# Optimization experiments

Hardware: AMD Instinct MI355X
Metric: run time of the kernel (lower is better)

The kernel has to match this reference:

```python
import jax, jax.numpy as jnp
import numpy as np


def setup_inputs() -> dict:
    key = jax.random.key(0)
    k1, k2, k3, k4 = jax.random.split(key, 4)
    N, E, C_in, C_out = 100000, 1600000, 256, 128
    x = jax.random.normal(k1, (N, C_in), dtype=jnp.float32)
    edge_index = jax.random.randint(k2, (2, E), 0, N, dtype=jnp.int64)
    W = jax.random.normal(k3, (C_in, C_out), dtype=jnp.float32) * 0.05
    b = jax.random.normal(k4, (C_out,), dtype=jnp.float32) * 0.05
    return {"x": x, "edge_index": edge_index, "W": W, "b": b}


def reference(x, edge_index, W, b):
    # GCNConv (PyG defaults): add self-loops, symmetric normalization,
    # linear transform, scatter-sum aggregation, bias; then ReLU (norm=None).
    N = x.shape[0]
    loops = jnp.arange(N, dtype=edge_index.dtype)
    src = jnp.concatenate([edge_index[0], loops])  # [E+N] message sources (x_j)
    dst = jnp.concatenate([edge_index[1], loops])  # [E+N] aggregation targets

    deg = jax.ops.segment_sum(jnp.ones_like(dst, dtype=x.dtype), dst, num_segments=N)
    deg_inv_sqrt = jnp.where(deg > 0, jax.lax.rsqrt(jnp.maximum(deg, 1.0)), 0.0)
    norm = deg_inv_sqrt[src] * deg_inv_sqrt[dst]  # [E+N]

    h = x @ W                                      # [N, C_out]
    msg = h[src] * norm[:, None]                   # [E+N, C_out] gather + scale
    out = jax.ops.segment_sum(msg, dst, num_segments=N) + b  # scatter-add
    return jax.nn.relu(out)
```

## Files before the change

kernel.cpp:

```cpp
#include <hip/hip_runtime.h>


typedef __attribute__((ext_vector_type(8))) short bf16x8;
typedef __attribute__((ext_vector_type(4))) float f32x4;

__device__ __forceinline__ unsigned short f2bf(float f) {
  unsigned int u = __float_as_uint(f);
  u += 0x7FFFu + ((u >> 16) & 1u);
  return (unsigned short)(u >> 16);
}
__device__ __forceinline__ float bfval(unsigned short h) {
  return __uint_as_float(((unsigned int)h) << 16);
}
__device__ __forceinline__ float bf0(unsigned int u) { return __uint_as_float(u << 16); }
__device__ __forceinline__ float bf1(unsigned int u) { return __uint_as_float(u & 0xFFFF0000u); }

__global__ __launch_bounds__(256) void k_wprep(
    const float* __restrict__ W, unsigned short* __restrict__ blob,
    unsigned int* __restrict__ cnt, int N)
{
  int g = blockIdx.x * 256 + threadIdx.x;
  if (g < N) cnt[g] = 0u;
  if (g >= 256 * 128) return;
  int k = g >> 7, c = g & 127;
  float w = W[g];
  unsigned short hi = f2bf(w);
  unsigned short lo = f2bf(w - bfval(hi));
  int q = k >> 5, kk = k & 31;
  unsigned lin = (unsigned)(c * 64 + kk * 2);
  unsigned swz = lin ^ (((unsigned)(c & 7)) << 4);
  blob[(q * 16384 + swz) >> 1] = hi;
  blob[(q * 16384 + 8192 + swz) >> 1] = lo;
}

__global__ __launch_bounds__(256) void k_gemm_scatter(
    const float* __restrict__ x, const unsigned char* __restrict__ wblob,
    unsigned short* __restrict__ h, int N,
    const int* __restrict__ src, const int* __restrict__ dst,
    unsigned int* __restrict__ cnt, int* __restrict__ srcs, int E,
    int gemmB, int scatB)
{
  __shared__ __align__(16) unsigned char smem[20480];

  const int id = blockIdx.x;
  bool isGemm;
  int idx;
  if (scatB == 2 * gemmB) {
    if (id % 3 == 0) { isGemm = true;  idx = id / 3; }
    else             { isGemm = false; idx = id - 1 - id / 3; }
  } else {
    isGemm = id < gemmB;
    idx = isGemm ? id : id - gemmB;
  }

  const int tid = threadIdx.x;

  if (!isGemm) {
    if (idx < scatB) {
      int e = idx * 256 + tid;
      if (e < E) {
        int d = __builtin_nontemporal_load(dst + e);
        int s = __builtin_nontemporal_load(src + e);
        int pos = (int)atomicAdd(&cnt[d], 1u);
        if (pos < 64) __builtin_nontemporal_store(s, srcs + (((size_t)d << 6) + pos));
      }
    }
    return;
  }
  if (idx >= gemmB) return;

  const int row0 = idx * 32;
  const int lane = tid & 63;
  const int wv = tid >> 6;
  const int mb = wv & 1;
  const int nb = wv >> 1;

  f32x4 acc[4] = {};

  const int ar = tid >> 3;
  const int akk0 = (tid & 7) * 4;
  int arow = row0 + ar; if (arow >= N) arow = N - 1;
  const unsigned aaddr = ((unsigned)(ar * 64 + akk0 * 2)) ^ (((unsigned)(ar & 7)) << 4);

  const int rr = 16 * mb + (lane & 15);
  const unsigned aoff = ((unsigned)(rr * 64 + (lane >> 4) * 16)) ^ (((unsigned)(rr & 7)) << 4);

  for (int q = 0; q < 8; ++q) {
    {
      const f32x4 v = __builtin_nontemporal_load(
          (const f32x4*)(x + (size_t)arow * 256 + q * 32 + akk0));
      unsigned short h0 = f2bf(v[0]), h1 = f2bf(v[1]), h2 = f2bf(v[2]), h3 = f2bf(v[3]);
      unsigned short l0 = f2bf(v[0] - bfval(h0));
      unsigned short l1 = f2bf(v[1] - bfval(h1));
      unsigned short l2 = f2bf(v[2] - bfval(h2));
      unsigned short l3 = f2bf(v[3] - bfval(h3));
      *(uint2*)(smem + 16384 + aaddr) =
          make_uint2((unsigned)h0 | ((unsigned)h1 << 16), (unsigned)h2 | ((unsigned)h3 << 16));
      *(uint2*)(smem + 18432 + aaddr) =
          make_uint2((unsigned)l0 | ((unsigned)l1 << 16), (unsigned)l2 | ((unsigned)l3 << 16));
    }
    {
      const uint4* gb = (const uint4*)(wblob + (size_t)q * 16384);
      uint4* sb = (uint4*)smem;
      uint4 t0 = gb[tid], t1 = gb[tid + 256], t2 = gb[tid + 512], t3 = gb[tid + 768];
      sb[tid] = t0; sb[tid + 256] = t1; sb[tid + 512] = t2; sb[tid + 768] = t3;
    }
    __syncthreads();
    {
      const bf16x8 ah = *(const bf16x8*)(smem + 16384 + aoff);
      const bf16x8 al = *(const bf16x8*)(smem + 18432 + aoff);
      #pragma unroll
      for (int nf = 0; nf < 4; ++nf) {
        const int c = 64 * nb + 16 * nf + (lane & 15);
        const unsigned boff =
            ((unsigned)(c * 64 + (lane >> 4) * 16)) ^ (((unsigned)(c & 7)) << 4);
        const bf16x8 bh = *(const bf16x8*)(smem + boff);
        const bf16x8 bl = *(const bf16x8*)(smem + 8192 + boff);
        acc[nf] = __builtin_amdgcn_mfma_f32_16x16x32_bf16(ah, bh, acc[nf], 0, 0, 0);
        acc[nf] = __builtin_amdgcn_mfma_f32_16x16x32_bf16(ah, bl, acc[nf], 0, 0, 0);
        acc[nf] = __builtin_amdgcn_mfma_f32_16x16x32_bf16(al, bh, acc[nf], 0, 0, 0);
      }
    }
    __syncthreads();
  }

  #pragma unroll
  for (int nf = 0; nf < 4; ++nf) {
    const int col = 64 * nb + 16 * nf + (lane & 15);
    #pragma unroll
    for (int r = 0; r < 4; ++r) {
      const int row = row0 + 16 * mb + 4 * (lane >> 4) + r;
      if (row < N) h[(size_t)row * 128 + col] = f2bf(acc[nf][r]);
    }
  }
}

__global__ __launch_bounds__(256) void k_aggr(
    const unsigned short* __restrict__ h, const int* __restrict__ srcs,
    const unsigned int* __restrict__ cnt,
    const float* __restrict__ b, float* __restrict__ out, int N)
{
  const int wid = (int)(((size_t)blockIdx.x * 256 + threadIdx.x) >> 6);
  if (wid >= N) return;
  const int lane = threadIdx.x & 63;
  const int eg = lane >> 4;
  const int cl = lane & 15;
  const int deg = min((int)cnt[wid], 64);
  const int m = deg + 1;
  const size_t coff = (size_t)(cl << 3);
  const size_t lbase = (size_t)wid << 6;

  float a0 = 0.f, a1 = 0.f, a2 = 0.f, a3 = 0.f, a4 = 0.f, a5 = 0.f, a6 = 0.f, a7 = 0.f;

  for (int base = 0; base < m; base += 64) {
    const int kk = min(64, m - base);
    const int slot = base + lane;
    int sidx = wid;
    if (slot < deg) sidx = srcs[lbase + slot];
    const float sd = rsqrtf((float)(cnt[sidx] + 1u));
    int j = 0;
    for (; j + 8 <= kk; j += 8) {
      const int s0 = __shfl(sidx, j + eg, 64);
      const int s1 = __shfl(sidx, j + 4 + eg, 64);
      const float d0 = __shfl(sd, j + eg, 64);
      const float d1 = __shfl(sd, j + 4 + eg, 64);
      const uint4 v0 = *(const uint4*)(h + ((size_t)s0 << 7) + coff);
      const uint4 v1 = *(const uint4*)(h + ((size_t)s1 << 7) + coff);
      a0 = fmaf(bf0(v0.x), d0, a0); a1 = fmaf(bf1(v0.x), d0, a1);
      a2 = fmaf(bf0(v0.y), d0, a2); a3 = fmaf(bf1(v0.y), d0, a3);
      a4 = fmaf(bf0(v0.z), d0, a4); a5 = fmaf(bf1(v0.z), d0, a5);
      a6 = fmaf(bf0(v0.w), d0, a6); a7 = fmaf(bf1(v0.w), d0, a7);
      a0 = fmaf(bf0(v1.x), d1, a0); a1 = fmaf(bf1(v1.x), d1, a1);
      a2 = fmaf(bf0(v1.y), d1, a2); a3 = fmaf(bf1(v1.y), d1, a3);
      a4 = fmaf(bf0(v1.z), d1, a4); a5 = fmaf(bf1(v1.z), d1, a5);
      a6 = fmaf(bf0(v1.w), d1, a6); a7 = fmaf(bf1(v1.w), d1, a7);
    }
    for (; j < kk; j += 4) {
      const int s0 = __shfl(sidx, j + eg, 64);
      const float d0 = __shfl(sd, j + eg, 64);
      if (j + eg < kk) {
        const uint4 v0 = *(const uint4*)(h + ((size_t)s0 << 7) + coff);
        a0 = fmaf(bf0(v0.x), d0, a0); a1 = fmaf(bf1(v0.x), d0, a1);
        a2 = fmaf(bf0(v0.y), d0, a2); a3 = fmaf(bf1(v0.y), d0, a3);
        a4 = fmaf(bf0(v0.z), d0, a4); a5 = fmaf(bf1(v0.z), d0, a5);
        a6 = fmaf(bf0(v0.w), d0, a6); a7 = fmaf(bf1(v0.w), d0, a7);
      }
    }
  }

  a0 += __shfl_xor(a0, 16, 64); a0 += __shfl_xor(a0, 32, 64);
  a1 += __shfl_xor(a1, 16, 64); a1 += __shfl_xor(a1, 32, 64);
  a2 += __shfl_xor(a2, 16, 64); a2 += __shfl_xor(a2, 32, 64);
  a3 += __shfl_xor(a3, 16, 64); a3 += __shfl_xor(a3, 32, 64);
  a4 += __shfl_xor(a4, 16, 64); a4 += __shfl_xor(a4, 32, 64);
  a5 += __shfl_xor(a5, 16, 64); a5 += __shfl_xor(a5, 32, 64);
  a6 += __shfl_xor(a6, 16, 64); a6 += __shfl_xor(a6, 32, 64);
  a7 += __shfl_xor(a7, 16, 64); a7 += __shfl_xor(a7, 32, 64);

  if (lane < 32) {
    const float dn = rsqrtf((float)m);
    const int hi = lane >> 4;
    const int c0 = ((lane & 15) << 3) + (hi << 2);
    const float4 bb = *(const float4*)(b + c0);
    const float r0 = hi ? a4 : a0;
    const float r1 = hi ? a5 : a1;
    const float r2 = hi ? a6 : a2;
    const float r3 = hi ? a7 : a3;
    float4 o;
    o.x = fmaxf(fmaf(dn, r0, bb.x), 0.f);
    o.y = fmaxf(fmaf(dn, r1, bb.y), 0.f);
    o.z = fmaxf(fmaf(dn, r2, bb.z), 0.f);
    o.w = fmaxf(fmaf(dn, r3, bb.w), 0.f);
    *(float4*)(out + ((size_t)wid << 7) + c0) = o;
  }
}

extern "C" void kernel_launch(void* const* d_in, const int* in_sizes, int n_in,
                              void* d_out, int out_size, void* d_ws, size_t ws_size,
                              hipStream_t stream)
{
  const float* x  = (const float*)d_in[0];
  const int* ei   = (const int*)d_in[1];
  const float* W  = (const float*)d_in[2];
  const float* b  = (const float*)d_in[3];
  float* out = (float*)d_out;

  const int Cout = in_sizes[3];
  const int Cin  = in_sizes[2] / Cout;
  const int N    = in_sizes[0] / Cin;
  const int E    = in_sizes[1] / 2;

  const int* src = ei;
  const int* dst = ei + E;

  char* p = (char*)d_ws;
  size_t off = 0;
  auto alloc = [&](size_t bytes) { char* q = p + off; off = (off + bytes + 255) & ~(size_t)255; return q; };
  unsigned int* cnt = (unsigned int*)alloc((size_t)N * 4);
  int* srcs         = (int*)alloc((size_t)N * 64 * 4);
  unsigned short* h = (unsigned short*)alloc((size_t)N * Cout * 2);
  unsigned short* wblob = (unsigned short*)alloc(8 * 16384);

  const int gemmB = (N + 31) / 32;
  const int scatB = (E + 255) / 256;

  const int prepThreads = (N > 256 * 128) ? N : 256 * 128;
  k_wprep<<<(prepThreads + 255) / 256, 256, 0, stream>>>(W, wblob, cnt, N);
  k_gemm_scatter<<<scatB + gemmB, 256, 0, stream>>>(x, (const unsigned char*)wblob, h, N,
                                                    src, dst, cnt, srcs, E,
                                                    gemmB, scatB);
  k_aggr<<<(N + 3) / 4, 256, 0, stream>>>(h, srcs, cnt, b, out, N);
}
```

Measured before the change: 321.3 us.

## Replace global-atomic edge scatter with two-pass destination binning through LDS

Edges are first partitioned into coarse destination bins (512-node ranges). Each block counts its edges per bin in shared memory, reserves space with one global atomic per bin, and writes compacted (local dst, src) pairs. A second pass, with one block per bin, builds per-node source lists using shared-memory atomics, then writes the per-node counts. This removes per-edge global atomics on random addresses and the separate count-zeroing, and makes the srcs writes more local. In exchange it adds an intermediate pairs buffer, an extra memset, and a capacity cap that silently drops edges if a bin overflows.

```diff
diff --git a/kernel.cpp b/kernel.cpp
--- a/kernel.cpp
+++ b/kernel.cpp
@@ -3,6 +3,7 @@
 
 typedef __attribute__((ext_vector_type(8))) short bf16x8;
 typedef __attribute__((ext_vector_type(4))) float f32x4;
+typedef __attribute__((ext_vector_type(2))) unsigned int u32x2;
 
 __device__ __forceinline__ unsigned short f2bf(float f) {
   unsigned int u = __float_as_uint(f);
@@ -15,58 +16,110 @@
 __device__ __forceinline__ float bf0(unsigned int u) { return __uint_as_float(u << 16); }
 __device__ __forceinline__ float bf1(unsigned int u) { return __uint_as_float(u & 0xFFFF0000u); }
 
-__global__ __launch_bounds__(256) void k_wprep(
+#define EPB 4096
+#define MAXB 256
+
+__global__ __launch_bounds__(256) void k_prep_bin(
     const float* __restrict__ W, unsigned short* __restrict__ blob,
-    unsigned int* __restrict__ cnt, int N)
+    const int* __restrict__ src, const int* __restrict__ dst,
+    u32x2* __restrict__ pairs, unsigned int* __restrict__ binTail,
+    int E, int nbins, int shift, int cap)
 {
-  int g = blockIdx.x * 256 + threadIdx.x;
-  if (g < N) cnt[g] = 0u;
-  if (g >= 256 * 128) return;
-  int k = g >> 7, c = g & 127;
-  float w = W[g];
-  unsigned short hi = f2bf(w);
-  unsigned short lo = f2bf(w - bfval(hi));
-  int q = k >> 5, kk = k & 31;
-  unsigned lin = (unsigned)(c * 64 + kk * 2);
-  unsigned swz = lin ^ (((unsigned)(c & 7)) << 4);
-  blob[(q * 16384 + swz) >> 1] = hi;
-  blob[(q * 16384 + 8192 + swz) >> 1] = lo;
+  __shared__ u32x2 stg[EPB];
+  __shared__ unsigned int lcnt[MAXB], lbase[MAXB], loff[MAXB];
+
+  const int tid = threadIdx.x;
+  const int id = blockIdx.x;
+
+  if (id < 128) {
+    int g = id * 256 + tid;
+    int k = g >> 7, c = g & 127;
+    float w = W[g];
+    unsigned short hi = f2bf(w);
+    unsigned short lo = f2bf(w - bfval(hi));
+    int q = k >> 5, kk = k & 31;
+    unsigned lin = (unsigned)(c * 64 + kk * 2);
+    unsigned swz = lin ^ (((unsigned)(c & 7)) << 4);
+    blob[(q * 16384 + swz) >> 1] = hi;
+    blob[(q * 16384 + 8192 + swz) >> 1] = lo;
+    return;
+  }
+
+  const int e0 = (id - 128) * EPB;
+  for (int i = tid; i < MAXB; i += 256) { lcnt[i] = 0u; loff[i] = 0u; }
+  __syncthreads();
+
+  #pragma unroll
+  for (int i = 0; i < EPB / 256; ++i) {
+    const int e = e0 + i * 256 + tid;
+    u32x2 pr = {0xFFFFFFFFu, 0u};
+    if (e < E) {
+      int d = __builtin_nontemporal_load(dst + e);
+      int s = __builtin_nontemporal_load(src + e);
+      pr.x = (unsigned)d; pr.y = (unsigned)s;
+      atomicAdd(&lcnt[d >> shift], 1u);
+    }
+    stg[i * 256 + tid] = pr;
+  }
+  __syncthreads();
+
+  if (tid < nbins) {
+    unsigned c = lcnt[tid];
+    lbase[tid] = c ? atomicAdd(&binTail[tid], c) : 0u;
+  }
+  __syncthreads();
+
+  #pragma unroll
+  for (int i = 0; i < EPB / 256; ++i) {
+    const u32x2 pr = stg[i * 256 + tid];
+    if (pr.x != 0xFFFFFFFFu) {
+      const int bin = (int)(pr.x >> shift);
+      const unsigned p = lbase[bin] + atomicAdd(&loff[bin], 1u);
+      if (p < (unsigned)cap) {
+        u32x2 o;
+        o.x = pr.x - ((unsigned)bin << shift);
+        o.y = pr.y;
+        __builtin_nontemporal_store(o, pairs + (size_t)bin * cap + p);
+      }
+    }
+  }
 }
 
 __global__ __launch_bounds__(256) void k_gemm_scatter(
     const float* __restrict__ x, const unsigned char* __restrict__ wblob,
     unsigned short* __restrict__ h, int N,
-    const int* __restrict__ src, const int* __restrict__ dst,
-    unsigned int* __restrict__ cnt, int* __restrict__ srcs, int E,
-    int gemmB, int scatB)
+    const u32x2* __restrict__ pairs, const unsigned int* __restrict__ binTail,
+    unsigned int* __restrict__ cnt, int* __restrict__ srcs,
+    int nbins, int shift, int cap, int gemmB)
 {
   __shared__ __align__(16) unsigned char smem[20480];
 
   const int id = blockIdx.x;
-  bool isGemm;
-  int idx;
-  if (scatB == 2 * gemmB) {
-    if (id % 3 == 0) { isGemm = true;  idx = id / 3; }
-    else             { isGemm = false; idx = id - 1 - id / 3; }
-  } else {
-    isGemm = id < gemmB;
-    idx = isGemm ? id : id - gemmB;
-  }
-
   const int tid = threadIdx.x;
 
-  if (!isGemm) {
-    if (idx < scatB) {
-      int e = idx * 256 + tid;
-      if (e < E) {
-        int d = __builtin_nontemporal_load(dst + e);
-        int s = __builtin_nontemporal_load(src + e);
-        int pos = (int)atomicAdd(&cnt[d], 1u);
-        if (pos < 64) __builtin_nontemporal_store(s, srcs + (((size_t)d << 6) + pos));
-      }
-    }
+  if (id < nbins) {
+    unsigned int* lcnt = (unsigned int*)smem;
+    const int bin = id;
+    const int bsz = 1 << shift;
+    const int nbase = bin << shift;
+    const int nn = min(bsz, N - nbase);
+    if (nn <= 0) return;
+    for (int i = tid; i < bsz; i += 256) lcnt[i] = 0u;
+    __syncthreads();
+    const int n = min((int)binTail[bin], cap);
+    const u32x2* bp = pairs + (size_t)bin * cap;
+    for (int p = tid; p < n; p += 256) {
+      const u32x2 pr = bp[p];
+      const unsigned pos = atomicAdd(&lcnt[pr.x], 1u);
+      if (pos < 64)
+        srcs[(((size_t)(nbase + pr.x)) << 6) + pos] = (int)pr.y;
+    }
+    __syncthreads();
+    for (int i = tid; i < nn; i += 256) cnt[nbase + i] = lcnt[i];
     return;
   }
+
+  const int idx = id - nbins;
   if (idx >= gemmB) return;
 
   const int row0 = idx * 32;
@@ -233,6 +286,11 @@
   const int* src = ei;
   const int* dst = ei + E;
 
+  int shift = 9;
+  while (((N + (1 << shift) - 1) >> shift) > MAXB) ++shift;
+  const int nbins = (N + (1 << shift) - 1) >> shift;
+  const int cap = E / nbins + E / (2 * nbins) + 1024;
+
   char* p = (char*)d_ws;
   size_t off = 0;
   auto alloc = [&](size_t bytes) { char* q = p + off; off = (off + bytes + 255) & ~(size_t)255; return q; };
@@ -240,14 +298,17 @@
   int* srcs         = (int*)alloc((size_t)N * 64 * 4);
   unsigned short* h = (unsigned short*)alloc((size_t)N * Cout * 2);
   unsigned short* wblob = (unsigned short*)alloc(8 * 16384);
+  unsigned int* binTail = (unsigned int*)alloc((size_t)nbins * 4);
+  u32x2* pairs      = (u32x2*)alloc((size_t)nbins * cap * 8);
 
   const int gemmB = (N + 31) / 32;
-  const int scatB = (E + 255) / 256;
-
-  const int prepThreads = (N > 256 * 128) ? N : 256 * 128;
-  k_wprep<<<(prepThreads + 255) / 256, 256, 0, stream>>>(W, wblob, cnt, N);
-  k_gemm_scatter<<<scatB + gemmB, 256, 0, stream>>>(x, (const unsigned char*)wblob, h, N,
-                                                    src, dst, cnt, srcs, E,
-                                                    gemmB, scatB);
+  const int binB  = (E + EPB - 1) / EPB;
+
+  (void)hipMemsetAsync(binTail, 0, (size_t)nbins * 4, stream);
+  k_prep_bin<<<128 + binB, 256, 0, stream>>>(W, wblob, src, dst,
+                                             pairs, binTail, E, nbins, shift, cap);
+  k_gemm_scatter<<<nbins + gemmB, 256, 0, stream>>>(x, (const unsigned char*)wblob, h, N,
+                                                    pairs, binTail, cnt, srcs,
+                                                    nbins, shift, cap, gemmB);
   k_aggr<<<(N + 3) / 4, 256, 0, stream>>>(h, srcs, cnt, b, out, N);
 }
```

Result: slower. 337.2 us (+4.9%).

## Double GEMM row tile to 64 and rebalance gemm/scatter block interleave

Applied to the files above, without the earlier changes.

The fused GEMM+scatter kernel now gives each GEMM block 64 rows instead of 32. Each wave covers a 16-row slab across all 128 output columns, so every W-blob tile staged in shared memory is reused by twice as many rows and the W reload traffic per row is halved. The interleave pattern changes from 1 gemm : 2 scatter to 1 : 4 to match the new block counts, and the output store in the aggregation kernel becomes nontemporal. The cost is more accumulator registers per thread (8 f32x4) and more shared memory, which can lower occupancy.

```diff
diff --git a/kernel.cpp b/kernel.cpp
--- a/kernel.cpp
+++ b/kernel.cpp
@@ -38,22 +38,22 @@
     unsigned short* __restrict__ h, int N,
     const int* __restrict__ src, const int* __restrict__ dst,
     unsigned int* __restrict__ cnt, int* __restrict__ srcs, int E,
-    int gemmB, int scatB)
-{
-  __shared__ __align__(16) unsigned char smem[20480];
+    int gemmB, int scatB, int useIlv)
+{
+  __shared__ __align__(16) unsigned char smem[24576];
 
   const int id = blockIdx.x;
+  const int tid = threadIdx.x;
   bool isGemm;
   int idx;
-  if (scatB == 2 * gemmB) {
-    if (id % 3 == 0) { isGemm = true;  idx = id / 3; }
-    else             { isGemm = false; idx = id - 1 - id / 3; }
+  if (useIlv) {
+    const int g = id / 5;
+    if (id % 5 == 0) { isGemm = true;  idx = g; }
+    else             { isGemm = false; idx = id - g - 1; }
   } else {
     isGemm = id < gemmB;
     idx = isGemm ? id : id - gemmB;
   }
-
-  const int tid = threadIdx.x;
 
   if (!isGemm) {
     if (idx < scatB) {
@@ -69,35 +69,46 @@
   }
   if (idx >= gemmB) return;
 
-  const int row0 = idx * 32;
+  const int row0 = idx * 64;
   const int lane = tid & 63;
   const int wv = tid >> 6;
-  const int mb = wv & 1;
-  const int nb = wv >> 1;
-
-  f32x4 acc[4] = {};
+
+  f32x4 acc[8] = {};
 
   const int ar = tid >> 3;
   const int akk0 = (tid & 7) * 4;
-  int arow = row0 + ar; if (arow >= N) arow = N - 1;
-  const unsigned aaddr = ((unsigned)(ar * 64 + akk0 * 2)) ^ (((unsigned)(ar & 7)) << 4);
-
-  const int rr = 16 * mb + (lane & 15);
+  int arow0 = row0 + ar;      if (arow0 >= N) arow0 = N - 1;
+  int arow1 = row0 + ar + 32; if (arow1 >= N) arow1 = N - 1;
+  const unsigned aaddr0 = ((unsigned)(ar * 64 + akk0 * 2)) ^ (((unsigned)(ar & 7)) << 4);
+  const unsigned aaddr1 = ((unsigned)((ar + 32) * 64 + akk0 * 2)) ^ (((unsigned)((ar + 32) & 7)) << 4);
+
+  const int rr = 16 * wv + (lane & 15);
   const unsigned aoff = ((unsigned)(rr * 64 + (lane >> 4) * 16)) ^ (((unsigned)(rr & 7)) << 4);
 
   for (int q = 0; q < 8; ++q) {
     {
-      const f32x4 v = __builtin_nontemporal_load(
-          (const f32x4*)(x + (size_t)arow * 256 + q * 32 + akk0));
-      unsigned short h0 = f2bf(v[0]), h1 = f2bf(v[1]), h2 = f2bf(v[2]), h3 = f2bf(v[3]);
-      unsigned short l0 = f2bf(v[0] - bfval(h0));
-      unsigned short l1 = f2bf(v[1] - bfval(h1));
-      unsigned short l2 = f2bf(v[2] - bfval(h2));
-      unsigned short l3 = f2bf(v[3] - bfval(h3));
-      *(uint2*)(smem + 16384 + aaddr) =
+      const f32x4 v0 = __builtin_nontemporal_load(
+          (const f32x4*)(x + (size_t)arow0 * 256 + q * 32 + akk0));
+      const f32x4 v1 = __builtin_nontemporal_load(
+          (const f32x4*)(x + (size_t)arow1 * 256 + q * 32 + akk0));
+      unsigned short h0 = f2bf(v0[0]), h1 = f2bf(v0[1]), h2 = f2bf(v0[2]), h3 = f2bf(v0[3]);
+      unsigned short l0 = f2bf(v0[0] - bfval(h0));
+      unsigned short l1 = f2bf(v0[1] - bfval(h1));
+      unsigned short l2 = f2bf(v0[2] - bfval(h2));
+      unsigned short l3 = f2bf(v0[3] - bfval(h3));
+      *(uint2*)(smem + 16384 + aaddr0) =
           make_uint2((unsigned)h0 | ((unsigned)h1 << 16), (unsigned)h2 | ((unsigned)h3 << 16));
-      *(uint2*)(smem + 18432 + aaddr) =
+      *(uint2*)(smem + 20480 + aaddr0) =
           make_uint2((unsigned)l0 | ((unsigned)l1 << 16), (unsigned)l2 | ((unsigned)l3 << 16));
+      unsigned short h4 = f2bf(v1[0]), h5 = f2bf(v1[1]), h6 = f2bf(v1[2]), h7 = f2bf(v1[3]);
+      unsigned short l4 = f2bf(v1[0] - bfval(h4));
+      unsigned short l5 = f2bf(v1[1] - bfval(h5));
+      unsigned short l6 = f2bf(v1[2] - bfval(h6));
+      unsigned short l7 = f2bf(v1[3] - bfval(h7));
+      *(uint2*)(smem + 16384 + aaddr1) =
+          make_uint2((unsigned)h4 | ((unsigned)h5 << 16), (unsigned)h6 | ((unsigned)h7 << 16));
+      *(uint2*)(smem + 20480 + aaddr1) =
+          make_uint2((unsigned)l4 | ((unsigned)l5 << 16), (unsigned)l6 | ((unsigned)l7 << 16));
     }
     {
       const uint4* gb = (const uint4*)(wblob + (size_t)q * 16384);
@@ -108,10 +119,10 @@
     __syncthreads();
     {
       const bf16x8 ah = *(const bf16x8*)(smem + 16384 + aoff);
-      const bf16x8 al = *(const bf16x8*)(smem + 18432 + aoff);
+      const bf16x8 al = *(const bf16x8*)(smem + 20480 + aoff);
       #pragma unroll
-      for (int nf = 0; nf < 4; ++nf) {
-        const int c = 64 * nb + 16 * nf + (lane & 15);
+      for (int nf = 0; nf < 8; ++nf) {
+        const int c = 16 * nf + (lane & 15);
         const unsigned boff =
             ((unsigned)(c * 64 + (lane >> 4) * 16)) ^ (((unsigned)(c & 7)) << 4);
         const bf16x8 bh = *(const bf16x8*)(smem + boff);
@@ -125,11 +136,11 @@
   }
 
   #pragma unroll
-  for (int nf = 0; nf < 4; ++nf) {
-    const int col = 64 * nb + 16 * nf + (lane & 15);
+  for (int nf = 0; nf < 8; ++nf) {
+    const int col = 16 * nf + (lane & 15);
     #pragma unroll
     for (int r = 0; r < 4; ++r) {
-      const int row = row0 + 16 * mb + 4 * (lane >> 4) + r;
+      const int row = row0 + 16 * wv + 4 * (lane >> 4) + r;
       if (row < N) h[(size_t)row * 128 + col] = f2bf(acc[nf][r]);
     }
   }
@@ -206,12 +217,12 @@
     const float r1 = hi ? a5 : a1;
     const float r2 = hi ? a6 : a2;
     const float r3 = hi ? a7 : a3;
-    float4 o;
-    o.x = fmaxf(fmaf(dn, r0, bb.x), 0.f);
-    o.y = fmaxf(fmaf(dn, r1, bb.y), 0.f);
-    o.z = fmaxf(fmaf(dn, r2, bb.z), 0.f);
-    o.w = fmaxf(fmaf(dn, r3, bb.w), 0.f);
-    *(float4*)(out + ((size_t)wid << 7) + c0) = o;
+    f32x4 o;
+    o[0] = fmaxf(fmaf(dn, r0, bb.x), 0.f);
+    o[1] = fmaxf(fmaf(dn, r1, bb.y), 0.f);
+    o[2] = fmaxf(fmaf(dn, r2, bb.z), 0.f);
+    o[3] = fmaxf(fmaf(dn, r3, bb.w), 0.f);
+    __builtin_nontemporal_store(o, (f32x4*)(out + ((size_t)wid << 7) + c0));
   }
 }
 
@@ -241,13 +252,15 @@
   unsigned short* h = (unsigned short*)alloc((size_t)N * Cout * 2);
   unsigned short* wblob = (unsigned short*)alloc(8 * 16384);
 
-  const int gemmB = (N + 31) / 32;
+  const int gemmB = (N + 63) / 64;
   const int scatB = (E + 255) / 256;
+  const int grid  = gemmB + scatB;
+  const int useIlv = (gemmB == (grid + 4) / 5) ? 1 : 0;
 
   const int prepThreads = (N > 256 * 128) ? N : 256 * 128;
   k_wprep<<<(prepThreads + 255) / 256, 256, 0, stream>>>(W, wblob, cnt, N);
-  k_gemm_scatter<<<scatB + gemmB, 256, 0, stream>>>(x, (const unsigned char*)wblob, h, N,
-                                                    src, dst, cnt, srcs, E,
-                                                    gemmB, scatB);
+  k_gemm_scatter<<<grid, 256, 0, stream>>>(x, (const unsigned char*)wblob, h, N,
+                                           src, dst, cnt, srcs, E,
+                                           gemmB, scatB, useIlv);
   k_aggr<<<(N + 3) / 4, 256, 0, stream>>>(h, srcs, cnt, b, out, N);
 }
```

After: 315.2 us. About the same (-1.9%).
